# Optimization experiments

Hardware: AMD Instinct MI355X
Metric: run time of the kernel (lower is better)

The kernel has to match this reference:

```python
import jax, jax.numpy as jnp
import numpy as np

B, P, K = 32, 2048, 16
NHID, NCLS = 128, 10

def setup_inputs() -> dict:
    key = jax.random.key(0)
    ks = jax.random.split(key, 8)
    def w(k, shape):
        fan_in = shape[0]
        return jax.random.normal(k, shape, jnp.float32) / np.sqrt(fan_in)
    pos = jax.random.normal(ks[0], (B * P, 3), jnp.float32)
    batch = jnp.repeat(jnp.arange(B, dtype=jnp.int32), P)
    return dict(
        pos=pos, batch=batch,
        W1a=w(ks[1], (3 + 3, NHID)), b1a=jnp.zeros((NHID,), jnp.float32),
        W1b=w(ks[2], (NHID, NHID)), b1b=jnp.zeros((NHID,), jnp.float32),
        W2a=w(ks[3], (NHID + 3, NHID)), b2a=jnp.zeros((NHID,), jnp.float32),
        W2b=w(ks[4], (NHID, NHID)), b2b=jnp.zeros((NHID,), jnp.float32),
        Wc=w(ks[5], (NHID, NCLS)), bc=jnp.zeros((NCLS,), jnp.float32),
    )

def _gather(x, idx):
    # x: [B,P,C], idx: [B,P,K] -> [B,P,K,C]
    return jax.vmap(lambda xb, ib: xb[ib])(x, idx)

def _knn(posb):
    # posb: [B,P,3]; k nearest (incl. self, loop=True) per node -> [B,P,K]
    sq = jnp.sum(posb * posb, axis=-1)                      # [B,P]
    d2 = sq[:, :, None] + sq[:, None, :] - 2.0 * jnp.einsum('bpd,bqd->bpq', posb, posb)
    _, nbr = jax.lax.top_k(-d2, K)                          # [B,P,K]
    return nbr

def _pointnet_layer(h, posb, nbr, Wa, ba, Wb, bb):
    # message: concat(h_j, pos_j - pos_i) -> Linear -> ReLU -> Linear; aggr = max over K
    h_j = _gather(h, nbr)                                   # [B,P,K,C]
    rel = _gather(posb, nbr) - posb[:, :, None, :]          # [B,P,K,3]
    m = jnp.concatenate([h_j, rel], axis=-1)                # [B,P,K,C+3]
    m = jax.nn.relu(jnp.einsum('bpkc,cd->bpkd', m, Wa) + ba)
    m = jnp.einsum('bpkc,cd->bpkd', m, Wb) + bb
    return jnp.max(m, axis=2)                               # [B,P,NHID]

def reference(pos, batch, W1a, b1a, W1b, b1b, W2a, b2a, W2b, b2b, Wc, bc):
    posb = pos.reshape(B, P, 3)                             # batch is sorted, equal-size graphs
    nbr = _knn(posb)
    h = jax.nn.relu(_pointnet_layer(posb, posb, nbr, W1a, b1a, W1b, b1b))
    h = jax.nn.relu(_pointnet_layer(h, posb, nbr, W2a, b2a, W2b, b2b))
    g = jnp.max(h, axis=1)                                  # global_max_pool -> [B,NHID]
    return g @ Wc + bc                                      # [B,NCLS]
```

## Files before the change

kernel.cpp:

```cpp
#include <hip/hip_runtime.h>


typedef __bf16 bf16x8 __attribute__((ext_vector_type(8)));
typedef float  f32x4  __attribute__((ext_vector_type(4)));

#define LDSA __attribute__((aligned(16)))
#define WAVE_LDS_SYNC() __asm__ volatile("s_waitcnt lgkmcnt(0)" ::: "memory")

__global__ __launch_bounds__(512, 4) void knn_kernel(const float* __restrict__ pos,
                                                     int* __restrict__ nbr) {
  __shared__ LDSA float4 P4[2048];
  const int blk = blockIdx.x;
  const int b = blk >> 5;
  const int tid = threadIdx.x;
  const size_t bbase = (size_t)b * 2048;
  for (int idx = tid; idx < 2048; idx += 512) {
    const float* pp = pos + (bbase + idx) * 3;
    float x = pp[0], y = pp[1], z = pp[2];
    P4[idx] = make_float4(x, y, z, fmaf(z, z, fmaf(y, y, x * x)));
  }
  __syncthreads();
  const int wave = tid >> 6, lane = tid & 63;
  const int p0 = (blk & 31) * 64 + wave * 8;
  const unsigned long long below = (1ull << lane) - 1ull;
  const float FINF = __uint_as_float(0x7F800000u);
  for (int it = 0; it < 8; ++it) {
    const int pl = p0 + it;
    const float4 P = P4[pl];
    float m1 = FINF, m2 = FINF, m3 = FINF;
    unsigned s1 = 0, s2 = 0, s3 = 0;
#pragma unroll 8
    for (int i = 0; i < 32; ++i) {
      int c = lane + (i << 6);
      float4 Q = P4[c];
      float d2 = (P.w + Q.w) - 2.0f * fmaf(P.z, Q.z, fmaf(P.y, Q.y, P.x * Q.x));
      bool c3 = d2 < m3, c2 = d2 < m2, c1 = d2 < m1;
      m3 = c2 ? m2 : (c3 ? d2 : m3);  s3 = c2 ? s2 : (c3 ? (unsigned)c : s3);
      m2 = c1 ? m1 : (c2 ? d2 : m2);  s2 = c1 ? s1 : (c2 ? (unsigned)c : s2);
      m1 = c1 ? d2 : m1;              s1 = c1 ? (unsigned)c : s1;
    }
    unsigned k1 = __float_as_uint(m1); k1 = ((int)k1 < 0) ? ~k1 : (k1 | 0x80000000u);
    unsigned k2 = __float_as_uint(m2); k2 = ((int)k2 < 0) ? ~k2 : (k2 | 0x80000000u);
    unsigned k3 = __float_as_uint(m3); k3 = ((int)k3 < 0) ? ~k3 : (k3 | 0x80000000u);
    unsigned v = 0;
#pragma unroll
    for (int bit = 31; bit >= 0; --bit) {
      unsigned t = v | (1u << bit);
      int cnt = __popcll(__ballot(k1 < t)) + __popcll(__ballot(k2 < t)) +
                __popcll(__ballot(k3 < t));
      if (cnt < 16) v = t;
    }
    const unsigned V = v;
    const long long outbase = ((long long)bbase + pl) * 16;
    if (__any(k3 < V)) {
      unsigned long long K1 = ((unsigned long long)k1 << 32) | s1;
      unsigned long long K2 = ((unsigned long long)k2 << 32) | s2;
      unsigned long long K3 = ((unsigned long long)k3 << 32) | s3;
      unsigned long long lastk = 0;
      for (int r = 0; r < 16; ++r) {
        unsigned long long k = K1, kmin = K1;
#pragma unroll
        for (int off = 1; off < 64; off <<= 1) {
          unsigned long long o = __shfl_xor(kmin, off);
          kmin = (o < kmin) ? o : kmin;
        }
        if (lane == r) nbr[outbase + r] = (int)(kmin & 0xFFFFFFFFull);
        if (k == kmin) { lastk = k; K1 = K2; K2 = K3; K3 = ~0ull; }
        if (r < 15 && __any(K1 == ~0ull)) {
          if (K1 == ~0ull) {
            unsigned long long best = ~0ull;
            for (int i = 0; i < 32; ++i) {
              int c = lane + (i << 6);
              float4 Q = P4[c];
              float d2 = (P.w + Q.w) - 2.0f * fmaf(P.z, Q.z, fmaf(P.y, Q.y, P.x * Q.x));
              unsigned u = __float_as_uint(d2);
              u = ((int)u < 0) ? ~u : (u | 0x80000000u);
              unsigned long long kc = ((unsigned long long)u << 32) | (unsigned)c;
              bool ok = (kc > lastk) & (kc < best);
              best = ok ? kc : best;
            }
            K1 = best;
          }
        }
      }
    } else {
      unsigned long long L1 = __ballot(k1 < V), L2 = __ballot(k2 < V), L3 = __ballot(k3 < V);
      unsigned long long E1 = __ballot(k1 == V), E2 = __ballot(k2 == V), E3 = __ballot(k3 == V);
      int cA = __popcll(L1), cB = cA + __popcll(L2), cT = cB + __popcll(L3);
      int eA = __popcll(E1), eB = eA + __popcll(E2);
      {
        bool lt = k1 < V, eq = k1 == V;
        int plt = __popcll(L1 & below);
        int peq = cT + __popcll(E1 & below);
        int p = lt ? plt : peq;
        if (lt || (eq && peq < 16)) nbr[outbase + p] = (int)s1;
      }
      {
        bool lt = k2 < V, eq = k2 == V;
        int plt = cA + __popcll(L2 & below);
        int peq = cT + eA + __popcll(E2 & below);
        int p = lt ? plt : peq;
        if (lt || (eq && peq < 16)) nbr[outbase + p] = (int)s2;
      }
      {
        bool lt = k3 < V, eq = k3 == V;
        int plt = cB + __popcll(L3 & below);
        int peq = cT + eB + __popcll(E3 & below);
        int p = lt ? plt : peq;
        if (lt || (eq && peq < 16)) nbr[outbase + p] = (int)s3;
      }
    }
  }
}

__global__ __launch_bounds__(256, 2) void layer1_kernel(
    const float* __restrict__ pos, const int* __restrict__ nbr,
    const float* __restrict__ W1a, const float* __restrict__ b1a,
    const float* __restrict__ W1b, const float* __restrict__ b1b,
    __bf16* __restrict__ h1e) {
  __shared__ LDSA char smem[34816];
  __bf16* Wbt = (__bf16*)smem;
  const int tid = threadIdx.x;
  for (int idx = tid; idx < 16384; idx += 256) {
    int k = idx >> 7, n = idx & 127;
    Wbt[n * 136 + k] = (__bf16)W1b[idx];
  }
  __syncthreads();
  const int wave = tid >> 6, lane = tid & 63;
  const int q = lane >> 4, c15 = lane & 15;
  bf16x8 bfr[8][4];
#pragma unroll
  for (int nt = 0; nt < 8; ++nt)
#pragma unroll
    for (int t = 0; t < 4; ++t)
      bfr[nt][t] = *(const bf16x8*)&Wbt[(nt * 16 + c15) * 136 + t * 32 + q * 8];
  __syncthreads();
  __bf16* mt = (__bf16*)smem + wave * 2176;
  float* base = (float*)(smem + 17408) + wave * 128;
  const int cb = lane & 7, k0 = lane >> 3, C0 = cb * 16;
  float4 s0h[4], s1h[4], s2h[4];
#pragma unroll
  for (int i = 0; i < 4; ++i) {
    float4 a0 = *(const float4*)&W1a[      C0 + 4 * i], r0 = *(const float4*)&W1a[384 + C0 + 4 * i];
    float4 a1 = *(const float4*)&W1a[128 + C0 + 4 * i], r1 = *(const float4*)&W1a[512 + C0 + 4 * i];
    float4 a2 = *(const float4*)&W1a[256 + C0 + 4 * i], r2 = *(const float4*)&W1a[640 + C0 + 4 * i];
    s0h[i] = make_float4(a0.x + r0.x, a0.y + r0.y, a0.z + r0.z, a0.w + r0.w);
    s1h[i] = make_float4(a1.x + r1.x, a1.y + r1.y, a1.z + r1.z, a1.w + r1.w);
    s2h[i] = make_float4(a2.x + r2.x, a2.y + r2.y, a2.z + r2.z, a2.w + r2.w);
  }
  const int c2 = lane * 2;
  const float br0a = W1a[384 + c2], br0b = W1a[384 + c2 + 1];
  const float br1a = W1a[512 + c2], br1b = W1a[512 + c2 + 1];
  const float br2a = W1a[640 + c2], br2b = W1a[640 + c2 + 1];
  const float ba0 = b1a[c2], ba1 = b1a[c2 + 1];
  const float bbi0 = b1b[q * 32 + c15], bbi1 = b1b[q * 32 + 16 + c15];
  const int blk = blockIdx.x, b = blk >> 5;
  const size_t bbase = (size_t)b * 2048;
  const int p0 = (blk & 31) * 64 + wave * 16;
  size_t node = bbase + p0;
  int j0 = nbr[node * 16 + k0];
  int j1 = nbr[node * 16 + k0 + 8];
  float px = pos[node * 3], py = pos[node * 3 + 1], pz = pos[node * 3 + 2];
  for (int it = 0; it < 16; ++it) {
    const int j0c = j0, j1c = j1;
    const float xp = px, yp = py, zp = pz;
    const size_t nodec = node;
    if (it < 15) {
      node = nodec + 1;
      j0 = nbr[node * 16 + k0];
      j1 = nbr[node * 16 + k0 + 8];
      px = pos[node * 3]; py = pos[node * 3 + 1]; pz = pos[node * 3 + 2];
    }
    const float* pj0 = pos + (bbase + j0c) * 3;
    const float* pj1 = pos + (bbase + j1c) * 3;
    const float xa = pj0[0], ya = pj0[1], za = pj0[2];
    const float xb = pj1[0], yb = pj1[1], zb = pj1[2];
    float v0 = ba0 - fmaf(xp, br0a, fmaf(yp, br1a, zp * br2a));
    float v1 = ba1 - fmaf(xp, br0b, fmaf(yp, br1b, zp * br2b));
    *(float2*)&base[c2] = make_float2(v0, v1);
    WAVE_LDS_SYNC();
    float4 bb[4];
#pragma unroll
    for (int i = 0; i < 4; ++i) bb[i] = *(const float4*)&base[C0 + 4 * i];
#pragma unroll
    for (int r = 0; r < 2; ++r) {
      const float xj = r ? xb : xa, yj = r ? yb : ya, zj = r ? zb : za;
      bf16x8 o0, o1;
#pragma unroll
      for (int i = 0; i < 4; ++i) {
        float mx = fmaf(xj, s0h[i].x, fmaf(yj, s1h[i].x, fmaf(zj, s2h[i].x, bb[i].x)));
        float my = fmaf(xj, s0h[i].y, fmaf(yj, s1h[i].y, fmaf(zj, s2h[i].y, bb[i].y)));
        float mz = fmaf(xj, s0h[i].z, fmaf(yj, s1h[i].z, fmaf(zj, s2h[i].z, bb[i].z)));
        float mw = fmaf(xj, s0h[i].w, fmaf(yj, s1h[i].w, fmaf(zj, s2h[i].w, bb[i].w)));
        __bf16 e0 = (__bf16)fmaxf(mx, 0.f), e1 = (__bf16)fmaxf(my, 0.f);
        __bf16 e2 = (__bf16)fmaxf(mz, 0.f), e3 = (__bf16)fmaxf(mw, 0.f);
        if (i < 2) { o0[i * 4 + 0] = e0; o0[i * 4 + 1] = e1; o0[i * 4 + 2] = e2; o0[i * 4 + 3] = e3; }
        else { o1[(i - 2) * 4 + 0] = e0; o1[(i - 2) * 4 + 1] = e1; o1[(i - 2) * 4 + 2] = e2; o1[(i - 2) * 4 + 3] = e3; }
      }
      __bf16* dst = &mt[(k0 + 8 * r) * 136 + C0];
      *(bf16x8*)dst = o0;
      *(bf16x8*)(dst + 8) = o1;
    }
    WAVE_LDS_SYNC();
    bf16x8 af[4];
#pragma unroll
    for (int t = 0; t < 4; ++t)
      af[t] = *(const bf16x8*)&mt[c15 * 136 + t * 32 + q * 8];
    f32x4 acc[8] = {};
#pragma unroll
    for (int nt = 0; nt < 8; ++nt)
#pragma unroll
      for (int t = 0; t < 4; ++t)
        acc[nt] = __builtin_amdgcn_mfma_f32_16x16x32_bf16(af[t], bfr[nt][t], acc[nt], 0, 0, 0);
#pragma unroll
    for (int nt = 0; nt < 8; ++nt) {
      float m4 = fmaxf(fmaxf(acc[nt][0], acc[nt][1]), fmaxf(acc[nt][2], acc[nt][3]));
      m4 = fmaxf(m4, __shfl_xor(m4, 16));
      m4 = fmaxf(m4, __shfl_xor(m4, 32));
      if ((nt >> 1) == q) {
        float bias = (nt & 1) ? bbi1 : bbi0;
        h1e[nodec * 160 + nt * 16 + c15] = (__bf16)fmaxf(m4 + bias, 0.f);
      }
    }
    if (lane < 32) {
      __bf16 v = (__bf16)0.f;
      if (lane == 0) v = (__bf16)xp;
      else if (lane == 1) v = (__bf16)yp;
      else if (lane == 2) v = (__bf16)zp;
      h1e[nodec * 160 + 128 + lane] = v;
    }
  }
}

__global__ __launch_bounds__(256) void mid_gemm_kernel(
    const __bf16* __restrict__ h1e, const float* __restrict__ W2a,
    const float* __restrict__ b2a, __bf16* __restrict__ u2p) {
  __shared__ LDSA __bf16 Wt[128 * 168];
  const int tid = threadIdx.x;
  uint4 z = make_uint4(0, 0, 0, 0);
  for (int idx = tid; idx < 2688; idx += 256) ((uint4*)Wt)[idx] = z;
  __syncthreads();
  for (int idx = tid; idx < 131 * 32; idx += 256) {
    int k = idx >> 5, c4 = (idx & 31) * 4;
    float4 w = *(const float4*)&W2a[k * 128 + c4];
    Wt[(c4 + 0) * 168 + k] = (__bf16)w.x;
    Wt[(c4 + 1) * 168 + k] = (__bf16)w.y;
    Wt[(c4 + 2) * 168 + k] = (__bf16)w.z;
    Wt[(c4 + 3) * 168 + k] = (__bf16)w.w;
  }
  const int wave = tid >> 6, lane = tid & 63;
  const int q = lane >> 4, c15 = lane & 15;
  float biasr[8];
#pragma unroll
  for (int nt = 0; nt < 8; ++nt) biasr[nt] = b2a[nt * 16 + c15];
  __syncthreads();
  for (int tile = 0; tile < 4; ++tile) {
    const int row0 = blockIdx.x * 256 + tile * 64 + wave * 16;
    bf16x8 af[5];
#pragma unroll
    for (int t = 0; t < 5; ++t)
      af[t] = *(const bf16x8*)(h1e + (size_t)(row0 + c15) * 160 + t * 32 + q * 8);
    f32x4 acc[8] = {};
#pragma unroll
    for (int nt = 0; nt < 8; ++nt)
#pragma unroll
      for (int t = 0; t < 5; ++t) {
        bf16x8 bf = *(const bf16x8*)&Wt[(nt * 16 + c15) * 168 + t * 32 + q * 8];
        acc[nt] = __builtin_amdgcn_mfma_f32_16x16x32_bf16(af[t], bf, acc[nt], 0, 0, 0);
      }
#pragma unroll
    for (int nt = 0; nt < 8; ++nt) {
#pragma unroll
      for (int r = 0; r < 4; ++r)
        u2p[(size_t)(row0 + q * 4 + r) * 128 + nt * 16 + c15] = (__bf16)(acc[nt][r] + biasr[nt]);
    }
  }
}

__global__ __launch_bounds__(256, 2) void layer2_kernel(
    const float* __restrict__ pos, const int* __restrict__ nbr,
    const __bf16* __restrict__ u2p, const float* __restrict__ W2a,
    const float* __restrict__ W2b, const float* __restrict__ b2b,
    int* __restrict__ gG) {
  __shared__ LDSA char smem[34816];
  __shared__ int gpart[128];
  __bf16* Wbt = (__bf16*)smem;
  const int tid = threadIdx.x;
  for (int idx = tid; idx < 16384; idx += 256) {
    int k = idx >> 7, n = idx & 127;
    Wbt[n * 136 + k] = (__bf16)W2b[idx];
  }
  if (tid < 128) gpart[tid] = 0;
  __syncthreads();
  const int wave = tid >> 6, lane = tid & 63;
  const int q = lane >> 4, c15 = lane & 15;
  bf16x8 bfr[8][4];
#pragma unroll
  for (int nt = 0; nt < 8; ++nt)
#pragma unroll
    for (int t = 0; t < 4; ++t)
      bfr[nt][t] = *(const bf16x8*)&Wbt[(nt * 16 + c15) * 136 + t * 32 + q * 8];
  __syncthreads();
  __bf16* mt = (__bf16*)smem + wave * 2176;
  float* proj = (float*)(smem + 17408) + wave * 128;
  const int cb = lane & 7, k0 = lane >> 3, C0 = cb * 16;
  const int c2 = lane * 2;
  const float r0a = W2a[16384 + c2], r0b = W2a[16384 + c2 + 1];
  const float r1a = W2a[16512 + c2], r1b = W2a[16512 + c2 + 1];
  const float r2a = W2a[16640 + c2], r2b = W2a[16640 + c2 + 1];
  const float bbi0 = b2b[q * 32 + c15], bbi1 = b2b[q * 32 + 16 + c15];
  const int lb = blockIdx.x;
  const int xcd = lb & 7, slot = lb >> 3;
  const int b = xcd + 8 * (slot >> 5);
  const int bi = slot & 31;
  const size_t bbase = (size_t)b * 2048;
  const int p0 = bi * 64 + wave * 16;
  size_t node = bbase + p0;
  int j0 = nbr[node * 16 + k0];
  int j1 = nbr[node * 16 + k0 + 8];
  float px = pos[node * 3], py = pos[node * 3 + 1], pz = pos[node * 3 + 2];
  for (int it = 0; it < 16; ++it) {
    const int j0c = j0, j1c = j1;
    const float xp = px, yp = py, zp = pz;
    const size_t nodec = node;
    if (it < 15) {
      node = nodec + 1;
      j0 = nbr[node * 16 + k0];
      j1 = nbr[node * 16 + k0 + 8];
      px = pos[node * 3]; py = pos[node * 3 + 1]; pz = pos[node * 3 + 2];
    }
    const __bf16* ur0 = u2p + (size_t)(bbase + j0c) * 128 + C0;
    const __bf16* ur1 = u2p + (size_t)(bbase + j1c) * 128 + C0;
    bf16x8 ua0 = *(const bf16x8*)ur0, ua1 = *(const bf16x8*)(ur0 + 8);
    bf16x8 ub0 = *(const bf16x8*)ur1, ub1 = *(const bf16x8*)(ur1 + 8);
    float v0 = fmaf(xp, r0a, fmaf(yp, r1a, zp * r2a));
    float v1 = fmaf(xp, r0b, fmaf(yp, r1b, zp * r2b));
    *(float2*)&proj[c2] = make_float2(v0, v1);
    WAVE_LDS_SYNC();
    float pj[16];
#pragma unroll
    for (int i = 0; i < 4; ++i) *(float4*)&pj[4 * i] = *(const float4*)&proj[C0 + 4 * i];
#pragma unroll
    for (int r = 0; r < 2; ++r) {
      bf16x8 u0 = r ? ub0 : ua0, u1 = r ? ub1 : ua1;
      bf16x8 o0, o1;
#pragma unroll
      for (int e = 0; e < 8; ++e) o0[e] = (__bf16)fmaxf((float)u0[e] - pj[e], 0.f);
#pragma unroll
      for (int e = 0; e < 8; ++e) o1[e] = (__bf16)fmaxf((float)u1[e] - pj[8 + e], 0.f);
      __bf16* dst = &mt[(k0 + 8 * r) * 136 + C0];
      *(bf16x8*)dst = o0;
      *(bf16x8*)(dst + 8) = o1;
    }
    WAVE_LDS_SYNC();
    bf16x8 af[4];
#pragma unroll
    for (int t = 0; t < 4; ++t)
      af[t] = *(const bf16x8*)&mt[c15 * 136 + t * 32 + q * 8];
    f32x4 acc[8] = {};
#pragma unroll
    for (int nt = 0; nt < 8; ++nt)
#pragma unroll
      for (int t = 0; t < 4; ++t)
        acc[nt] = __builtin_amdgcn_mfma_f32_16x16x32_bf16(af[t], bfr[nt][t], acc[nt], 0, 0, 0);
#pragma unroll
    for (int nt = 0; nt < 8; ++nt) {
      float m4 = fmaxf(fmaxf(acc[nt][0], acc[nt][1]), fmaxf(acc[nt][2], acc[nt][3]));
      m4 = fmaxf(m4, __shfl_xor(m4, 16));
      m4 = fmaxf(m4, __shfl_xor(m4, 32));
      if ((nt >> 1) == q) {
        float bias = (nt & 1) ? bbi1 : bbi0;
        float h = fmaxf(m4 + bias, 0.f);
        atomicMax(&gpart[nt * 16 + c15], __float_as_int(h));
      }
    }
  }
  __syncthreads();
  if (tid < 128) atomicMax(&gG[b * 128 + tid], gpart[tid]);
}

__global__ __launch_bounds__(64) void cls_kernel(const int* __restrict__ gG,
                                                 const float* __restrict__ Wc,
                                                 const float* __restrict__ bc,
                                                 float* __restrict__ out) {
  const int b = blockIdx.x, lane = threadIdx.x;
  float g1 = __int_as_float(gG[b * 128 + lane]);
  float g2 = __int_as_float(gG[b * 128 + 64 + lane]);
  float accn[10];
#pragma unroll
  for (int n = 0; n < 10; ++n)
    accn[n] = g1 * Wc[lane * 10 + n] + g2 * Wc[(64 + lane) * 10 + n];
#pragma unroll
  for (int n = 0; n < 10; ++n) {
#pragma unroll
    for (int off = 32; off >= 1; off >>= 1) accn[n] += __shfl_xor(accn[n], off);
  }
  if (lane == 0) {
#pragma unroll
    for (int n = 0; n < 10; ++n) out[b * 10 + n] = accn[n] + bc[n];
  }
}

extern "C" void kernel_launch(void* const* d_in, const int* in_sizes, int n_in,
                              void* d_out, int out_size, void* d_ws, size_t ws_size,
                              hipStream_t stream) {
  const float* pos = (const float*)d_in[0];
  const float* W1a = (const float*)d_in[2];
  const float* b1a = (const float*)d_in[3];
  const float* W1b = (const float*)d_in[4];
  const float* b1b = (const float*)d_in[5];
  const float* W2a = (const float*)d_in[6];
  const float* b2a = (const float*)d_in[7];
  const float* W2b = (const float*)d_in[8];
  const float* b2b = (const float*)d_in[9];
  const float* Wc  = (const float*)d_in[10];
  const float* bc  = (const float*)d_in[11];

  char* ws = (char*)d_ws;
  int*    nbr = (int*)ws;
  __bf16* h1e = (__bf16*)(ws + 4194304);
  __bf16* u2p = (__bf16*)(ws + 25165824);
  int*    gG  = (int*)(ws + 41943040);
  float*  out = (float*)d_out;

  hipMemsetAsync(gG, 0, 32 * 128 * sizeof(int), stream);
  knn_kernel<<<1024, 512, 0, stream>>>(pos, nbr);
  layer1_kernel<<<1024, 256, 0, stream>>>(pos, nbr, W1a, b1a, W1b, b1b, h1e);
  mid_gemm_kernel<<<256, 256, 0, stream>>>(h1e, W2a, b2a, u2p);
  layer2_kernel<<<1024, 256, 0, stream>>>(pos, nbr, u2p, W2a, W2b, b2b, gG);
  cls_kernel<<<32, 64, 0, stream>>>(gG, Wc, bc, out);
}
```

Measured before the change: 350.8 us.

## Process four query points per kNN pass and prefetch neighbor gathers one iteration ahead

The kNN kernel now handles four query points at once, so each candidate float4 loaded from LDS is reused for four distance computations. The radix-select ballots for the four points are interleaved to overlap their latency, and the occupancy hint of 4 blocks is removed from the launch bounds. Both layer kernels now software-pipeline the dependent gather (neighbor positions in layer 1, projected features in layer 2) one iteration ahead instead of issuing it right after the index load. This trades more registers, and possibly lower occupancy, for less LDS traffic and more hidden memory latency.

Result: slower. 385.0 us (+9.8%).

```diff
diff --git a/kernel.cpp b/kernel.cpp
--- a/kernel.cpp
+++ b/kernel.cpp
@@ -7,8 +7,8 @@
 #define LDSA __attribute__((aligned(16)))
 #define WAVE_LDS_SYNC() __asm__ volatile("s_waitcnt lgkmcnt(0)" ::: "memory")
 
-__global__ __launch_bounds__(512, 4) void knn_kernel(const float* __restrict__ pos,
-                                                     int* __restrict__ nbr) {
+__global__ __launch_bounds__(512) void knn_kernel(const float* __restrict__ pos,
+                                                  int* __restrict__ nbr) {
   __shared__ LDSA float4 P4[2048];
   const int blk = blockIdx.x;
   const int b = blk >> 5;
@@ -24,90 +24,109 @@
   const int p0 = (blk & 31) * 64 + wave * 8;
   const unsigned long long below = (1ull << lane) - 1ull;
   const float FINF = __uint_as_float(0x7F800000u);
-  for (int it = 0; it < 8; ++it) {
-    const int pl = p0 + it;
-    const float4 P = P4[pl];
-    float m1 = FINF, m2 = FINF, m3 = FINF;
-    unsigned s1 = 0, s2 = 0, s3 = 0;
-#pragma unroll 8
+  for (int g = 0; g < 2; ++g) {
+    const int pb = p0 + g * 4;
+    float4 Pp[4];
+#pragma unroll
+    for (int p = 0; p < 4; ++p) Pp[p] = P4[pb + p];
+    float m1[4], m2[4], m3[4];
+    unsigned s1[4], s2[4], s3[4];
+#pragma unroll
+    for (int p = 0; p < 4; ++p) { m1[p] = m2[p] = m3[p] = FINF; s1[p] = s2[p] = s3[p] = 0; }
+#pragma unroll 2
     for (int i = 0; i < 32; ++i) {
       int c = lane + (i << 6);
       float4 Q = P4[c];
-      float d2 = (P.w + Q.w) - 2.0f * fmaf(P.z, Q.z, fmaf(P.y, Q.y, P.x * Q.x));
-      bool c3 = d2 < m3, c2 = d2 < m2, c1 = d2 < m1;
-      m3 = c2 ? m2 : (c3 ? d2 : m3);  s3 = c2 ? s2 : (c3 ? (unsigned)c : s3);
-      m2 = c1 ? m1 : (c2 ? d2 : m2);  s2 = c1 ? s1 : (c2 ? (unsigned)c : s2);
-      m1 = c1 ? d2 : m1;              s1 = c1 ? (unsigned)c : s1;
-    }
-    unsigned k1 = __float_as_uint(m1); k1 = ((int)k1 < 0) ? ~k1 : (k1 | 0x80000000u);
-    unsigned k2 = __float_as_uint(m2); k2 = ((int)k2 < 0) ? ~k2 : (k2 | 0x80000000u);
-    unsigned k3 = __float_as_uint(m3); k3 = ((int)k3 < 0) ? ~k3 : (k3 | 0x80000000u);
-    unsigned v = 0;
-#pragma unroll
+#pragma unroll
+      for (int p = 0; p < 4; ++p) {
+        float d2 = (Pp[p].w + Q.w) - 2.0f * fmaf(Pp[p].z, Q.z, fmaf(Pp[p].y, Q.y, Pp[p].x * Q.x));
+        bool c3 = d2 < m3[p], c2 = d2 < m2[p], c1 = d2 < m1[p];
+        m3[p] = c2 ? m2[p] : (c3 ? d2 : m3[p]);  s3[p] = c2 ? s2[p] : (c3 ? (unsigned)c : s3[p]);
+        m2[p] = c1 ? m1[p] : (c2 ? d2 : m2[p]);  s2[p] = c1 ? s1[p] : (c2 ? (unsigned)c : s2[p]);
+        m1[p] = c1 ? d2 : m1[p];                 s1[p] = c1 ? (unsigned)c : s1[p];
+      }
+    }
+    unsigned k1[4], k2[4], k3[4];
+#pragma unroll
+    for (int p = 0; p < 4; ++p) {
+      unsigned u;
+      u = __float_as_uint(m1[p]); k1[p] = ((int)u < 0) ? ~u : (u | 0x80000000u);
+      u = __float_as_uint(m2[p]); k2[p] = ((int)u < 0) ? ~u : (u | 0x80000000u);
+      u = __float_as_uint(m3[p]); k3[p] = ((int)u < 0) ? ~u : (u | 0x80000000u);
+    }
+    unsigned v[4] = {0, 0, 0, 0};
     for (int bit = 31; bit >= 0; --bit) {
-      unsigned t = v | (1u << bit);
-      int cnt = __popcll(__ballot(k1 < t)) + __popcll(__ballot(k2 < t)) +
-                __popcll(__ballot(k3 < t));
-      if (cnt < 16) v = t;
-    }
-    const unsigned V = v;
-    const long long outbase = ((long long)bbase + pl) * 16;
-    if (__any(k3 < V)) {
-      unsigned long long K1 = ((unsigned long long)k1 << 32) | s1;
-      unsigned long long K2 = ((unsigned long long)k2 << 32) | s2;
-      unsigned long long K3 = ((unsigned long long)k3 << 32) | s3;
-      unsigned long long lastk = 0;
-      for (int r = 0; r < 16; ++r) {
-        unsigned long long k = K1, kmin = K1;
-#pragma unroll
-        for (int off = 1; off < 64; off <<= 1) {
-          unsigned long long o = __shfl_xor(kmin, off);
-          kmin = (o < kmin) ? o : kmin;
-        }
-        if (lane == r) nbr[outbase + r] = (int)(kmin & 0xFFFFFFFFull);
-        if (k == kmin) { lastk = k; K1 = K2; K2 = K3; K3 = ~0ull; }
-        if (r < 15 && __any(K1 == ~0ull)) {
-          if (K1 == ~0ull) {
-            unsigned long long best = ~0ull;
-            for (int i = 0; i < 32; ++i) {
-              int c = lane + (i << 6);
-              float4 Q = P4[c];
-              float d2 = (P.w + Q.w) - 2.0f * fmaf(P.z, Q.z, fmaf(P.y, Q.y, P.x * Q.x));
-              unsigned u = __float_as_uint(d2);
-              u = ((int)u < 0) ? ~u : (u | 0x80000000u);
-              unsigned long long kc = ((unsigned long long)u << 32) | (unsigned)c;
-              bool ok = (kc > lastk) & (kc < best);
-              best = ok ? kc : best;
+      const unsigned msk = 1u << bit;
+#pragma unroll
+      for (int p = 0; p < 4; ++p) {
+        unsigned t = v[p] | msk;
+        int cnt = __popcll(__ballot(k1[p] < t)) + __popcll(__ballot(k2[p] < t)) +
+                  __popcll(__ballot(k3[p] < t));
+        if (cnt < 16) v[p] = t;
+      }
+    }
+#pragma unroll 1
+    for (int p = 0; p < 4; ++p) {
+      const unsigned V = v[p];
+      const long long outbase = ((long long)bbase + pb + p) * 16;
+      if (__any(k3[p] < V)) {
+        unsigned long long K1 = ((unsigned long long)k1[p] << 32) | s1[p];
+        unsigned long long K2 = ((unsigned long long)k2[p] << 32) | s2[p];
+        unsigned long long K3 = ((unsigned long long)k3[p] << 32) | s3[p];
+        unsigned long long lastk = 0;
+        const float4 P = Pp[p];
+        for (int r = 0; r < 16; ++r) {
+          unsigned long long k = K1, kmin = K1;
+#pragma unroll
+          for (int off = 1; off < 64; off <<= 1) {
+            unsigned long long o = __shfl_xor(kmin, off);
+            kmin = (o < kmin) ? o : kmin;
+          }
+          if (lane == r) nbr[outbase + r] = (int)(kmin & 0xFFFFFFFFull);
+          if (k == kmin) { lastk = k; K1 = K2; K2 = K3; K3 = ~0ull; }
+          if (r < 15 && __any(K1 == ~0ull)) {
+            if (K1 == ~0ull) {
+              unsigned long long best = ~0ull;
+              for (int i = 0; i < 32; ++i) {
+                int c = lane + (i << 6);
+                float4 Q = P4[c];
+                float d2 = (P.w + Q.w) - 2.0f * fmaf(P.z, Q.z, fmaf(P.y, Q.y, P.x * Q.x));
+                unsigned u = __float_as_uint(d2);
+                u = ((int)u < 0) ? ~u : (u | 0x80000000u);
+                unsigned long long kc = ((unsigned long long)u << 32) | (unsigned)c;
+                bool ok = (kc > lastk) & (kc < best);
+                best = ok ? kc : best;
+              }
+              K1 = best;
             }
-            K1 = best;
           }
         }
-      }
-    } else {
-      unsigned long long L1 = __ballot(k1 < V), L2 = __ballot(k2 < V), L3 = __ballot(k3 < V);
-      unsigned long long E1 = __ballot(k1 == V), E2 = __ballot(k2 == V), E3 = __ballot(k3 == V);
-      int cA = __popcll(L1), cB = cA + __popcll(L2), cT = cB + __popcll(L3);
-      int eA = __popcll(E1), eB = eA + __popcll(E2);
-      {
-        bool lt = k1 < V, eq = k1 == V;
-        int plt = __popcll(L1 & below);
-        int peq = cT + __popcll(E1 & below);
-        int p = lt ? plt : peq;
-        if (lt || (eq && peq < 16)) nbr[outbase + p] = (int)s1;
-      }
-      {
-        bool lt = k2 < V, eq = k2 == V;
-        int plt = cA + __popcll(L2 & below);
-        int peq = cT + eA + __popcll(E2 & below);
-        int p = lt ? plt : peq;
-        if (lt || (eq && peq < 16)) nbr[outbase + p] = (int)s2;
-      }
-      {
-        bool lt = k3 < V, eq = k3 == V;
-        int plt = cB + __popcll(L3 & below);
-        int peq = cT + eB + __popcll(E3 & below);
-        int p = lt ? plt : peq;
-        if (lt || (eq && peq < 16)) nbr[outbase + p] = (int)s3;
+      } else {
+        unsigned long long L1 = __ballot(k1[p] < V), L2 = __ballot(k2[p] < V), L3 = __ballot(k3[p] < V);
+        unsigned long long E1 = __ballot(k1[p] == V), E2 = __ballot(k2[p] == V), E3 = __ballot(k3[p] == V);
+        int cA = __popcll(L1), cB = cA + __popcll(L2), cT = cB + __popcll(L3);
+        int eA = __popcll(E1), eB = eA + __popcll(E2);
+        {
+          bool lt = k1[p] < V, eq = k1[p] == V;
+          int plt = __popcll(L1 & below);
+          int peq = cT + __popcll(E1 & below);
+          int pp2 = lt ? plt : peq;
+          if (lt || (eq && peq < 16)) nbr[outbase + pp2] = (int)s1[p];
+        }
+        {
+          bool lt = k2[p] < V, eq = k2[p] == V;
+          int plt = cA + __popcll(L2 & below);
+          int peq = cT + eA + __popcll(E2 & below);
+          int pp2 = lt ? plt : peq;
+          if (lt || (eq && peq < 16)) nbr[outbase + pp2] = (int)s2[p];
+        }
+        {
+          bool lt = k3[p] < V, eq = k3[p] == V;
+          int plt = cB + __popcll(L3 & below);
+          int peq = cT + eB + __popcll(E3 & below);
+          int pp2 = lt ? plt : peq;
+          if (lt || (eq && peq < 16)) nbr[outbase + pp2] = (int)s3[p];
+        }
       }
     }
   }
@@ -161,20 +180,25 @@
   int j0 = nbr[node * 16 + k0];
   int j1 = nbr[node * 16 + k0 + 8];
   float px = pos[node * 3], py = pos[node * 3 + 1], pz = pos[node * 3 + 2];
+  const float* t0 = pos + (bbase + j0) * 3;
+  const float* t1 = pos + (bbase + j1) * 3;
+  float xa = t0[0], ya = t0[1], za = t0[2];
+  float xb = t1[0], yb = t1[1], zb = t1[2];
   for (int it = 0; it < 16; ++it) {
-    const int j0c = j0, j1c = j1;
     const float xp = px, yp = py, zp = pz;
+    const float xac = xa, yac = ya, zac = za;
+    const float xbc = xb, ybc = yb, zbc = zb;
     const size_t nodec = node;
     if (it < 15) {
       node = nodec + 1;
       j0 = nbr[node * 16 + k0];
       j1 = nbr[node * 16 + k0 + 8];
       px = pos[node * 3]; py = pos[node * 3 + 1]; pz = pos[node * 3 + 2];
-    }
-    const float* pj0 = pos + (bbase + j0c) * 3;
-    const float* pj1 = pos + (bbase + j1c) * 3;
-    const float xa = pj0[0], ya = pj0[1], za = pj0[2];
-    const float xb = pj1[0], yb = pj1[1], zb = pj1[2];
+      const float* n0 = pos + (bbase + j0) * 3;
+      const float* n1 = pos + (bbase + j1) * 3;
+      xa = n0[0]; ya = n0[1]; za = n0[2];
+      xb = n1[0]; yb = n1[1]; zb = n1[2];
+    }
     float v0 = ba0 - fmaf(xp, br0a, fmaf(yp, br1a, zp * br2a));
     float v1 = ba1 - fmaf(xp, br0b, fmaf(yp, br1b, zp * br2b));
     *(float2*)&base[c2] = make_float2(v0, v1);
@@ -184,7 +208,7 @@
     for (int i = 0; i < 4; ++i) bb[i] = *(const float4*)&base[C0 + 4 * i];
 #pragma unroll
     for (int r = 0; r < 2; ++r) {
-      const float xj = r ? xb : xa, yj = r ? yb : ya, zj = r ? zb : za;
+      const float xj = r ? xbc : xac, yj = r ? ybc : yac, zj = r ? zbc : zac;
       bf16x8 o0, o1;
 #pragma unroll
       for (int i = 0; i < 4; ++i) {
@@ -319,20 +343,24 @@
   int j0 = nbr[node * 16 + k0];
   int j1 = nbr[node * 16 + k0 + 8];
   float px = pos[node * 3], py = pos[node * 3 + 1], pz = pos[node * 3 + 2];
+  const __bf16* g0 = u2p + (size_t)(bbase + j0) * 128 + C0;
+  const __bf16* g1 = u2p + (size_t)(bbase + j1) * 128 + C0;
+  bf16x8 ua0 = *(const bf16x8*)g0, ua1 = *(const bf16x8*)(g0 + 8);
+  bf16x8 ub0 = *(const bf16x8*)g1, ub1 = *(const bf16x8*)(g1 + 8);
   for (int it = 0; it < 16; ++it) {
-    const int j0c = j0, j1c = j1;
     const float xp = px, yp = py, zp = pz;
+    const bf16x8 ua0c = ua0, ua1c = ua1, ub0c = ub0, ub1c = ub1;
     const size_t nodec = node;
     if (it < 15) {
       node = nodec + 1;
       j0 = nbr[node * 16 + k0];
       j1 = nbr[node * 16 + k0 + 8];
       px = pos[node * 3]; py = pos[node * 3 + 1]; pz = pos[node * 3 + 2];
-    }
-    const __bf16* ur0 = u2p + (size_t)(bbase + j0c) * 128 + C0;
-    const __bf16* ur1 = u2p + (size_t)(bbase + j1c) * 128 + C0;
-    bf16x8 ua0 = *(const bf16x8*)ur0, ua1 = *(const bf16x8*)(ur0 + 8);
-    bf16x8 ub0 = *(const bf16x8*)ur1, ub1 = *(const bf16x8*)(ur1 + 8);
+      const __bf16* n0 = u2p + (size_t)(bbase + j0) * 128 + C0;
+      const __bf16* n1 = u2p + (size_t)(bbase + j1) * 128 + C0;
+      ua0 = *(const bf16x8*)n0; ua1 = *(const bf16x8*)(n0 + 8);
+      ub0 = *(const bf16x8*)n1; ub1 = *(const bf16x8*)(n1 + 8);
+    }
     float v0 = fmaf(xp, r0a, fmaf(yp, r1a, zp * r2a));
     float v1 = fmaf(xp, r0b, fmaf(yp, r1b, zp * r2b));
     *(float2*)&proj[c2] = make_float2(v0, v1);
@@ -342,7 +370,7 @@
     for (int i = 0; i < 4; ++i) *(float4*)&pj[4 * i] = *(const float4*)&proj[C0 + 4 * i];
 #pragma unroll
     for (int r = 0; r < 2; ++r) {
-      bf16x8 u0 = r ? ub0 : ua0, u1 = r ? ub1 : ua1;
+      bf16x8 u0 = r ? ub0c : ua0c, u1 = r ? ub1c : ua1c;
       bf16x8 o0, o1;
 #pragma unroll
       for (int e = 0; e < 8; ++e) o0[e] = (__bf16)fmaxf((float)u0[e] - pj[e], 0.f);
```

## Process two query points per kNN pass and prefetch neighbor gathers one iteration ahead

Applied to the files above, without the earlier changes.

The kNN kernel now handles two query points per scan of the shared position array, so each LDS load of a candidate is reused for two distance computations. The two radix-select loops are interleaved, and the fallback and emit paths are moved into helper functions. In both PointNet layer kernels, the gathered neighbor data (positions or u2p rows) is now loaded one node ahead, so the dependent gather latency overlaps with the current iteration's compute. The cost is higher register pressure from the doubled top-3 state and the prefetched values, which may reduce occupancy.

Result: slower. 388.8 us (+10.8%).

```diff
diff --git a/kernel.cpp b/kernel.cpp
--- a/kernel.cpp
+++ b/kernel.cpp
@@ -6,6 +6,73 @@
 
 #define LDSA __attribute__((aligned(16)))
 #define WAVE_LDS_SYNC() __asm__ volatile("s_waitcnt lgkmcnt(0)" ::: "memory")
+
+__device__ __forceinline__ void knn_emit_set(
+    unsigned V, unsigned k1, unsigned s1, unsigned k2, unsigned s2,
+    unsigned k3, unsigned s3, unsigned long long below,
+    int* __restrict__ nbr, long long outbase) {
+  unsigned long long L1 = __ballot(k1 < V), L2 = __ballot(k2 < V), L3 = __ballot(k3 < V);
+  unsigned long long E1 = __ballot(k1 == V), E2 = __ballot(k2 == V), E3 = __ballot(k3 == V);
+  int cA = __popcll(L1), cB = cA + __popcll(L2), cT = cB + __popcll(L3);
+  int eA = __popcll(E1), eB = eA + __popcll(E2);
+  {
+    bool lt = k1 < V, eq = k1 == V;
+    int plt = __popcll(L1 & below);
+    int peq = cT + __popcll(E1 & below);
+    int p = lt ? plt : peq;
+    if (lt || (eq && peq < 16)) nbr[outbase + p] = (int)s1;
+  }
+  {
+    bool lt = k2 < V, eq = k2 == V;
+    int plt = cA + __popcll(L2 & below);
+    int peq = cT + eA + __popcll(E2 & below);
+    int p = lt ? plt : peq;
+    if (lt || (eq && peq < 16)) nbr[outbase + p] = (int)s2;
+  }
+  {
+    bool lt = k3 < V, eq = k3 == V;
+    int plt = cB + __popcll(L3 & below);
+    int peq = cT + eB + __popcll(E3 & below);
+    int p = lt ? plt : peq;
+    if (lt || (eq && peq < 16)) nbr[outbase + p] = (int)s3;
+  }
+}
+
+__device__ __forceinline__ void knn_fallback(
+    const float4* __restrict__ P4, float4 P, int lane,
+    unsigned k1, unsigned s1, unsigned k2, unsigned s2, unsigned k3, unsigned s3,
+    int* __restrict__ nbr, long long outbase) {
+  unsigned long long K1 = ((unsigned long long)k1 << 32) | s1;
+  unsigned long long K2 = ((unsigned long long)k2 << 32) | s2;
+  unsigned long long K3 = ((unsigned long long)k3 << 32) | s3;
+  unsigned long long lastk = 0;
+  for (int r = 0; r < 16; ++r) {
+    unsigned long long k = K1, kmin = K1;
+#pragma unroll
+    for (int off = 1; off < 64; off <<= 1) {
+      unsigned long long o = __shfl_xor(kmin, off);
+      kmin = (o < kmin) ? o : kmin;
+    }
+    if (lane == r) nbr[outbase + r] = (int)(kmin & 0xFFFFFFFFull);
+    if (k == kmin) { lastk = k; K1 = K2; K2 = K3; K3 = ~0ull; }
+    if (r < 15 && __any(K1 == ~0ull)) {
+      if (K1 == ~0ull) {
+        unsigned long long best = ~0ull;
+        for (int i = 0; i < 32; ++i) {
+          int c = lane + (i << 6);
+          float4 Q = P4[c];
+          float d2 = (P.w + Q.w) - 2.0f * fmaf(P.z, Q.z, fmaf(P.y, Q.y, P.x * Q.x));
+          unsigned u = __float_as_uint(d2);
+          u = ((int)u < 0) ? ~u : (u | 0x80000000u);
+          unsigned long long kc = ((unsigned long long)u << 32) | (unsigned)c;
+          bool ok = (kc > lastk) & (kc < best);
+          best = ok ? kc : best;
+        }
+        K1 = best;
+      }
+    }
+  }
+}
 
 __global__ __launch_bounds__(512, 4) void knn_kernel(const float* __restrict__ pos,
                                                      int* __restrict__ nbr) {
@@ -24,92 +91,61 @@
   const int p0 = (blk & 31) * 64 + wave * 8;
   const unsigned long long below = (1ull << lane) - 1ull;
   const float FINF = __uint_as_float(0x7F800000u);
-  for (int it = 0; it < 8; ++it) {
-    const int pl = p0 + it;
-    const float4 P = P4[pl];
-    float m1 = FINF, m2 = FINF, m3 = FINF;
-    unsigned s1 = 0, s2 = 0, s3 = 0;
-#pragma unroll 8
+  for (int g = 0; g < 4; ++g) {
+    const int pA = p0 + g * 2;
+    const float4 Pa = P4[pA];
+    const float4 Pb = P4[pA + 1];
+    float m1a = FINF, m2a = FINF, m3a = FINF, m1b = FINF, m2b = FINF, m3b = FINF;
+    unsigned s1a = 0, s2a = 0, s3a = 0, s1b = 0, s2b = 0, s3b = 0;
+#pragma unroll 4
     for (int i = 0; i < 32; ++i) {
       int c = lane + (i << 6);
       float4 Q = P4[c];
-      float d2 = (P.w + Q.w) - 2.0f * fmaf(P.z, Q.z, fmaf(P.y, Q.y, P.x * Q.x));
-      bool c3 = d2 < m3, c2 = d2 < m2, c1 = d2 < m1;
-      m3 = c2 ? m2 : (c3 ? d2 : m3);  s3 = c2 ? s2 : (c3 ? (unsigned)c : s3);
-      m2 = c1 ? m1 : (c2 ? d2 : m2);  s2 = c1 ? s1 : (c2 ? (unsigned)c : s2);
-      m1 = c1 ? d2 : m1;              s1 = c1 ? (unsigned)c : s1;
-    }
-    unsigned k1 = __float_as_uint(m1); k1 = ((int)k1 < 0) ? ~k1 : (k1 | 0x80000000u);
-    unsigned k2 = __float_as_uint(m2); k2 = ((int)k2 < 0) ? ~k2 : (k2 | 0x80000000u);
-    unsigned k3 = __float_as_uint(m3); k3 = ((int)k3 < 0) ? ~k3 : (k3 | 0x80000000u);
-    unsigned v = 0;
-#pragma unroll
+      float da = (Pa.w + Q.w) - 2.0f * fmaf(Pa.z, Q.z, fmaf(Pa.y, Q.y, Pa.x * Q.x));
+      float db = (Pb.w + Q.w) - 2.0f * fmaf(Pb.z, Q.z, fmaf(Pb.y, Q.y, Pb.x * Q.x));
+      {
+        bool c3 = da < m3a, c2 = da < m2a, c1 = da < m1a;
+        m3a = c2 ? m2a : (c3 ? da : m3a);  s3a = c2 ? s2a : (c3 ? (unsigned)c : s3a);
+        m2a = c1 ? m1a : (c2 ? da : m2a);  s2a = c1 ? s1a : (c2 ? (unsigned)c : s2a);
+        m1a = c1 ? da : m1a;               s1a = c1 ? (unsigned)c : s1a;
+      }
+      {
+        bool c3 = db < m3b, c2 = db < m2b, c1 = db < m1b;
+        m3b = c2 ? m2b : (c3 ? db : m3b);  s3b = c2 ? s2b : (c3 ? (unsigned)c : s3b);
+        m2b = c1 ? m1b : (c2 ? db : m2b);  s2b = c1 ? s1b : (c2 ? (unsigned)c : s2b);
+        m1b = c1 ? db : m1b;               s1b = c1 ? (unsigned)c : s1b;
+      }
+    }
+    unsigned u;
+    unsigned k1a, k2a, k3a, k1b, k2b, k3b;
+    u = __float_as_uint(m1a); k1a = ((int)u < 0) ? ~u : (u | 0x80000000u);
+    u = __float_as_uint(m2a); k2a = ((int)u < 0) ? ~u : (u | 0x80000000u);
+    u = __float_as_uint(m3a); k3a = ((int)u < 0) ? ~u : (u | 0x80000000u);
+    u = __float_as_uint(m1b); k1b = ((int)u < 0) ? ~u : (u | 0x80000000u);
+    u = __float_as_uint(m2b); k2b = ((int)u < 0) ? ~u : (u | 0x80000000u);
+    u = __float_as_uint(m3b); k3b = ((int)u < 0) ? ~u : (u | 0x80000000u);
+    unsigned va = 0, vb = 0;
     for (int bit = 31; bit >= 0; --bit) {
-      unsigned t = v | (1u << bit);
-      int cnt = __popcll(__ballot(k1 < t)) + __popcll(__ballot(k2 < t)) +
-                __popcll(__ballot(k3 < t));
-      if (cnt < 16) v = t;
-    }
-    const unsigned V = v;
-    const long long outbase = ((long long)bbase + pl) * 16;
-    if (__any(k3 < V)) {
-      unsigned long long K1 = ((unsigned long long)k1 << 32) | s1;
-      unsigned long long K2 = ((unsigned long long)k2 << 32) | s2;
-      unsigned long long K3 = ((unsigned long long)k3 << 32) | s3;
-      unsigned long long lastk = 0;
-      for (int r = 0; r < 16; ++r) {
-        unsigned long long k = K1, kmin = K1;
-#pragma unroll
-        for (int off = 1; off < 64; off <<= 1) {
-          unsigned long long o = __shfl_xor(kmin, off);
-          kmin = (o < kmin) ? o : kmin;
-        }
-        if (lane == r) nbr[outbase + r] = (int)(kmin & 0xFFFFFFFFull);
-        if (k == kmin) { lastk = k; K1 = K2; K2 = K3; K3 = ~0ull; }
-        if (r < 15 && __any(K1 == ~0ull)) {
-          if (K1 == ~0ull) {
-            unsigned long long best = ~0ull;
-            for (int i = 0; i < 32; ++i) {
-              int c = lane + (i << 6);
-              float4 Q = P4[c];
-              float d2 = (P.w + Q.w) - 2.0f * fmaf(P.z, Q.z, fmaf(P.y, Q.y, P.x * Q.x));
-              unsigned u = __float_as_uint(d2);
-              u = ((int)u < 0) ? ~u : (u | 0x80000000u);
-              unsigned long long kc = ((unsigned long long)u << 32) | (unsigned)c;
-              bool ok = (kc > lastk) & (kc < best);
-              best = ok ? kc : best;
-            }
-            K1 = best;
-          }
-        }
-      }
-    } else {
-      unsigned long long L1 = __ballot(k1 < V), L2 = __ballot(k2 < V), L3 = __ballot(k3 < V);
-      unsigned long long E1 = __ballot(k1 == V), E2 = __ballot(k2 == V), E3 = __ballot(k3 == V);
-      int cA = __popcll(L1), cB = cA + __popcll(L2), cT = cB + __popcll(L3);
-      int eA = __popcll(E1), eB = eA + __popcll(E2);
-      {
-        bool lt = k1 < V, eq = k1 == V;
-        int plt = __popcll(L1 & below);
-        int peq = cT + __popcll(E1 & below);
-        int p = lt ? plt : peq;
-        if (lt || (eq && peq < 16)) nbr[outbase + p] = (int)s1;
-      }
-      {
-        bool lt = k2 < V, eq = k2 == V;
-        int plt = cA + __popcll(L2 & below);
-        int peq = cT + eA + __popcll(E2 & below);
-        int p = lt ? plt : peq;
-        if (lt || (eq && peq < 16)) nbr[outbase + p] = (int)s2;
-      }
-      {
-        bool lt = k3 < V, eq = k3 == V;
-        int plt = cB + __popcll(L3 & below);
-        int peq = cT + eB + __popcll(E3 & below);
-        int p = lt ? plt : peq;
-        if (lt || (eq && peq < 16)) nbr[outbase + p] = (int)s3;
-      }
-    }
+      const unsigned msk = 1u << bit;
+      unsigned ta = va | msk;
+      int ca = __popcll(__ballot(k1a < ta)) + __popcll(__ballot(k2a < ta)) +
+               __popcll(__ballot(k3a < ta));
+      if (ca < 16) va = ta;
+      unsigned tb = vb | msk;
+      int cb2 = __popcll(__ballot(k1b < tb)) + __popcll(__ballot(k2b < tb)) +
+                __popcll(__ballot(k3b < tb));
+      if (cb2 < 16) vb = tb;
+    }
+    const long long outA = ((long long)bbase + pA) * 16;
+    const long long outB = outA + 16;
+    if (__any(k3a < va))
+      knn_fallback(P4, Pa, lane, k1a, s1a, k2a, s2a, k3a, s3a, nbr, outA);
+    else
+      knn_emit_set(va, k1a, s1a, k2a, s2a, k3a, s3a, below, nbr, outA);
+    if (__any(k3b < vb))
+      knn_fallback(P4, Pb, lane, k1b, s1b, k2b, s2b, k3b, s3b, nbr, outB);
+    else
+      knn_emit_set(vb, k1b, s1b, k2b, s2b, k3b, s3b, below, nbr, outB);
   }
 }
 
@@ -161,20 +197,25 @@
   int j0 = nbr[node * 16 + k0];
   int j1 = nbr[node * 16 + k0 + 8];
   float px = pos[node * 3], py = pos[node * 3 + 1], pz = pos[node * 3 + 2];
+  const float* t0 = pos + (bbase + j0) * 3;
+  const float* t1 = pos + (bbase + j1) * 3;
+  float xa = t0[0], ya = t0[1], za = t0[2];
+  float xb = t1[0], yb = t1[1], zb = t1[2];
   for (int it = 0; it < 16; ++it) {
-    const int j0c = j0, j1c = j1;
     const float xp = px, yp = py, zp = pz;
+    const float xac = xa, yac = ya, zac = za;
+    const float xbc = xb, ybc = yb, zbc = zb;
     const size_t nodec = node;
     if (it < 15) {
       node = nodec + 1;
       j0 = nbr[node * 16 + k0];
       j1 = nbr[node * 16 + k0 + 8];
       px = pos[node * 3]; py = pos[node * 3 + 1]; pz = pos[node * 3 + 2];
-    }
-    const float* pj0 = pos + (bbase + j0c) * 3;
-    const float* pj1 = pos + (bbase + j1c) * 3;
-    const float xa = pj0[0], ya = pj0[1], za = pj0[2];
-    const float xb = pj1[0], yb = pj1[1], zb = pj1[2];
+      const float* n0 = pos + (bbase + j0) * 3;
+      const float* n1 = pos + (bbase + j1) * 3;
+      xa = n0[0]; ya = n0[1]; za = n0[2];
+      xb = n1[0]; yb = n1[1]; zb = n1[2];
+    }
     float v0 = ba0 - fmaf(xp, br0a, fmaf(yp, br1a, zp * br2a));
     float v1 = ba1 - fmaf(xp, br0b, fmaf(yp, br1b, zp * br2b));
     *(float2*)&base[c2] = make_float2(v0, v1);
@@ -184,7 +225,7 @@
     for (int i = 0; i < 4; ++i) bb[i] = *(const float4*)&base[C0 + 4 * i];
 #pragma unroll
     for (int r = 0; r < 2; ++r) {
-      const float xj = r ? xb : xa, yj = r ? yb : ya, zj = r ? zb : za;
+      const float xj = r ? xbc : xac, yj = r ? ybc : yac, zj = r ? zbc : zac;
       bf16x8 o0, o1;
 #pragma unroll
       for (int i = 0; i < 4; ++i) {
@@ -319,20 +360,24 @@
   int j0 = nbr[node * 16 + k0];
   int j1 = nbr[node * 16 + k0 + 8];
   float px = pos[node * 3], py = pos[node * 3 + 1], pz = pos[node * 3 + 2];
+  const __bf16* g0 = u2p + (size_t)(bbase + j0) * 128 + C0;
+  const __bf16* g1 = u2p + (size_t)(bbase + j1) * 128 + C0;
+  bf16x8 ua0 = *(const bf16x8*)g0, ua1 = *(const bf16x8*)(g0 + 8);
+  bf16x8 ub0 = *(const bf16x8*)g1, ub1 = *(const bf16x8*)(g1 + 8);
   for (int it = 0; it < 16; ++it) {
-    const int j0c = j0, j1c = j1;
     const float xp = px, yp = py, zp = pz;
+    const bf16x8 ua0c = ua0, ua1c = ua1, ub0c = ub0, ub1c = ub1;
     const size_t nodec = node;
     if (it < 15) {
       node = nodec + 1;
       j0 = nbr[node * 16 + k0];
       j1 = nbr[node * 16 + k0 + 8];
       px = pos[node * 3]; py = pos[node * 3 + 1]; pz = pos[node * 3 + 2];
-    }
-    const __bf16* ur0 = u2p + (size_t)(bbase + j0c) * 128 + C0;
-    const __bf16* ur1 = u2p + (size_t)(bbase + j1c) * 128 + C0;
-    bf16x8 ua0 = *(const bf16x8*)ur0, ua1 = *(const bf16x8*)(ur0 + 8);
-    bf16x8 ub0 = *(const bf16x8*)ur1, ub1 = *(const bf16x8*)(ur1 + 8);
+      const __bf16* n0 = u2p + (size_t)(bbase + j0) * 128 + C0;
+      const __bf16* n1 = u2p + (size_t)(bbase + j1) * 128 + C0;
+      ua0 = *(const bf16x8*)n0; ua1 = *(const bf16x8*)(n0 + 8);
+      ub0 = *(const bf16x8*)n1; ub1 = *(const bf16x8*)(n1 + 8);
+    }
     float v0 = fmaf(xp, r0a, fmaf(yp, r1a, zp * r2a));
     float v1 = fmaf(xp, r0b, fmaf(yp, r1b, zp * r2b));
     *(float2*)&proj[c2] = make_float2(v0, v1);
@@ -342,7 +387,7 @@
     for (int i = 0; i < 4; ++i) *(float4*)&pj[4 * i] = *(const float4*)&proj[C0 + 4 * i];
 #pragma unroll
     for (int r = 0; r < 2; ++r) {
-      bf16x8 u0 = r ? ub0 : ua0, u1 = r ? ub1 : ua1;
+      bf16x8 u0 = r ? ub0c : ua0c, u1 = r ? ub1c : ua1c;
       bf16x8 o0, o1;
 #pragma unroll
       for (int e = 0; e < 8; ++e) o0[e] = (__bf16)fmaxf((float)u0[e] - pj[e], 0.f);
```

## Simplify kNN distance with med3 top-3 and prefetch gathered neighbor data

Applied to the files above, without the earlier changes.

The kNN kernel now stores -2*pos in LDS so each candidate distance is three chained FMAs, dropping the separate |p|^2 term, which is constant per query row and so leaves the ranking unchanged. The running top-3 minimum update uses fmed3/fmin instead of nested selects, and the launch_bounds min-occupancy hint is removed. In both pointnet layers, the dependent gather of neighbor positions and neighbor feature rows is software-pipelined one node ahead, so those loads overlap the current iteration's compute. This adds register pressure, and the distance values change numerically, which could reorder near-ties.

New measurement: 362.6 us. 1.03x slower.

```diff
diff --git a/kernel.cpp b/kernel.cpp
--- a/kernel.cpp
+++ b/kernel.cpp
@@ -7,8 +7,8 @@
 #define LDSA __attribute__((aligned(16)))
 #define WAVE_LDS_SYNC() __asm__ volatile("s_waitcnt lgkmcnt(0)" ::: "memory")
 
-__global__ __launch_bounds__(512, 4) void knn_kernel(const float* __restrict__ pos,
-                                                     int* __restrict__ nbr) {
+__global__ __launch_bounds__(512) void knn_kernel(const float* __restrict__ pos,
+                                                  int* __restrict__ nbr) {
   __shared__ LDSA float4 P4[2048];
   const int blk = blockIdx.x;
   const int b = blk >> 5;
@@ -17,7 +17,7 @@
   for (int idx = tid; idx < 2048; idx += 512) {
     const float* pp = pos + (bbase + idx) * 3;
     float x = pp[0], y = pp[1], z = pp[2];
-    P4[idx] = make_float4(x, y, z, fmaf(z, z, fmaf(y, y, x * x)));
+    P4[idx] = make_float4(-2.0f * x, -2.0f * y, -2.0f * z, fmaf(z, z, fmaf(y, y, x * x)));
   }
   __syncthreads();
   const int wave = tid >> 6, lane = tid & 63;
@@ -26,22 +26,29 @@
   const float FINF = __uint_as_float(0x7F800000u);
   for (int it = 0; it < 8; ++it) {
     const int pl = p0 + it;
-    const float4 P = P4[pl];
+    const float4 Qp = P4[pl];
+    const float Px = -0.5f * Qp.x, Py = -0.5f * Qp.y, Pz = -0.5f * Qp.z;
     float m1 = FINF, m2 = FINF, m3 = FINF;
     unsigned s1 = 0, s2 = 0, s3 = 0;
 #pragma unroll 8
     for (int i = 0; i < 32; ++i) {
       int c = lane + (i << 6);
       float4 Q = P4[c];
-      float d2 = (P.w + Q.w) - 2.0f * fmaf(P.z, Q.z, fmaf(P.y, Q.y, P.x * Q.x));
-      bool c3 = d2 < m3, c2 = d2 < m2, c1 = d2 < m1;
-      m3 = c2 ? m2 : (c3 ? d2 : m3);  s3 = c2 ? s2 : (c3 ? (unsigned)c : s3);
-      m2 = c1 ? m1 : (c2 ? d2 : m2);  s2 = c1 ? s1 : (c2 ? (unsigned)c : s2);
-      m1 = c1 ? d2 : m1;              s1 = c1 ? (unsigned)c : s1;
-    }
-    unsigned k1 = __float_as_uint(m1); k1 = ((int)k1 < 0) ? ~k1 : (k1 | 0x80000000u);
-    unsigned k2 = __float_as_uint(m2); k2 = ((int)k2 < 0) ? ~k2 : (k2 | 0x80000000u);
-    unsigned k3 = __float_as_uint(m3); k3 = ((int)k3 < 0) ? ~k3 : (k3 | 0x80000000u);
+      float d2 = fmaf(Px, Q.x, fmaf(Py, Q.y, fmaf(Pz, Q.z, Q.w)));
+      bool c1 = d2 < m1, c2 = d2 < m2, c3 = d2 < m3;
+      float n3 = __builtin_amdgcn_fmed3f(d2, m2, m3);
+      float n2 = __builtin_amdgcn_fmed3f(d2, m1, m2);
+      float n1 = fminf(d2, m1);
+      s3 = c2 ? s2 : (c3 ? (unsigned)c : s3);
+      s2 = c1 ? s1 : (c2 ? (unsigned)c : s2);
+      s1 = c1 ? (unsigned)c : s1;
+      m1 = n1; m2 = n2; m3 = n3;
+    }
+    unsigned u;
+    unsigned k1, k2, k3;
+    u = __float_as_uint(m1); k1 = ((int)u < 0) ? ~u : (u | 0x80000000u);
+    u = __float_as_uint(m2); k2 = ((int)u < 0) ? ~u : (u | 0x80000000u);
+    u = __float_as_uint(m3); k3 = ((int)u < 0) ? ~u : (u | 0x80000000u);
     unsigned v = 0;
 #pragma unroll
     for (int bit = 31; bit >= 0; --bit) {
@@ -72,10 +79,10 @@
             for (int i = 0; i < 32; ++i) {
               int c = lane + (i << 6);
               float4 Q = P4[c];
-              float d2 = (P.w + Q.w) - 2.0f * fmaf(P.z, Q.z, fmaf(P.y, Q.y, P.x * Q.x));
-              unsigned u = __float_as_uint(d2);
-              u = ((int)u < 0) ? ~u : (u | 0x80000000u);
-              unsigned long long kc = ((unsigned long long)u << 32) | (unsigned)c;
+              float d2 = fmaf(Px, Q.x, fmaf(Py, Q.y, fmaf(Pz, Q.z, Q.w)));
+              unsigned uu = __float_as_uint(d2);
+              uu = ((int)uu < 0) ? ~uu : (uu | 0x80000000u);
+              unsigned long long kc = ((unsigned long long)uu << 32) | (unsigned)c;
               bool ok = (kc > lastk) & (kc < best);
               best = ok ? kc : best;
             }
@@ -161,20 +168,25 @@
   int j0 = nbr[node * 16 + k0];
   int j1 = nbr[node * 16 + k0 + 8];
   float px = pos[node * 3], py = pos[node * 3 + 1], pz = pos[node * 3 + 2];
+  const float* t0 = pos + (bbase + j0) * 3;
+  const float* t1 = pos + (bbase + j1) * 3;
+  float xa = t0[0], ya = t0[1], za = t0[2];
+  float xb = t1[0], yb = t1[1], zb = t1[2];
   for (int it = 0; it < 16; ++it) {
-    const int j0c = j0, j1c = j1;
     const float xp = px, yp = py, zp = pz;
+    const float xac = xa, yac = ya, zac = za;
+    const float xbc = xb, ybc = yb, zbc = zb;
     const size_t nodec = node;
     if (it < 15) {
       node = nodec + 1;
       j0 = nbr[node * 16 + k0];
       j1 = nbr[node * 16 + k0 + 8];
       px = pos[node * 3]; py = pos[node * 3 + 1]; pz = pos[node * 3 + 2];
-    }
-    const float* pj0 = pos + (bbase + j0c) * 3;
-    const float* pj1 = pos + (bbase + j1c) * 3;
-    const float xa = pj0[0], ya = pj0[1], za = pj0[2];
-    const float xb = pj1[0], yb = pj1[1], zb = pj1[2];
+      const float* n0 = pos + (bbase + j0) * 3;
+      const float* n1 = pos + (bbase + j1) * 3;
+      xa = n0[0]; ya = n0[1]; za = n0[2];
+      xb = n1[0]; yb = n1[1]; zb = n1[2];
+    }
     float v0 = ba0 - fmaf(xp, br0a, fmaf(yp, br1a, zp * br2a));
     float v1 = ba1 - fmaf(xp, br0b, fmaf(yp, br1b, zp * br2b));
     *(float2*)&base[c2] = make_float2(v0, v1);
@@ -184,7 +196,7 @@
     for (int i = 0; i < 4; ++i) bb[i] = *(const float4*)&base[C0 + 4 * i];
 #pragma unroll
     for (int r = 0; r < 2; ++r) {
-      const float xj = r ? xb : xa, yj = r ? yb : ya, zj = r ? zb : za;
+      const float xj = r ? xbc : xac, yj = r ? ybc : yac, zj = r ? zbc : zac;
       bf16x8 o0, o1;
 #pragma unroll
       for (int i = 0; i < 4; ++i) {
@@ -319,20 +331,24 @@
   int j0 = nbr[node * 16 + k0];
   int j1 = nbr[node * 16 + k0 + 8];
   float px = pos[node * 3], py = pos[node * 3 + 1], pz = pos[node * 3 + 2];
+  const __bf16* g0 = u2p + (size_t)(bbase + j0) * 128 + C0;
+  const __bf16* g1 = u2p + (size_t)(bbase + j1) * 128 + C0;
+  bf16x8 ua0 = *(const bf16x8*)g0, ua1 = *(const bf16x8*)(g0 + 8);
+  bf16x8 ub0 = *(const bf16x8*)g1, ub1 = *(const bf16x8*)(g1 + 8);
   for (int it = 0; it < 16; ++it) {
-    const int j0c = j0, j1c = j1;
     const float xp = px, yp = py, zp = pz;
+    const bf16x8 ua0c = ua0, ua1c = ua1, ub0c = ub0, ub1c = ub1;
     const size_t nodec = node;
     if (it < 15) {
       node = nodec + 1;
       j0 = nbr[node * 16 + k0];
       j1 = nbr[node * 16 + k0 + 8];
       px = pos[node * 3]; py = pos[node * 3 + 1]; pz = pos[node * 3 + 2];
-    }
-    const __bf16* ur0 = u2p + (size_t)(bbase + j0c) * 128 + C0;
-    const __bf16* ur1 = u2p + (size_t)(bbase + j1c) * 128 + C0;
-    bf16x8 ua0 = *(const bf16x8*)ur0, ua1 = *(const bf16x8*)(ur0 + 8);
-    bf16x8 ub0 = *(const bf16x8*)ur1, ub1 = *(const bf16x8*)(ur1 + 8);
+      const __bf16* n0 = u2p + (size_t)(bbase + j0) * 128 + C0;
+      const __bf16* n1 = u2p + (size_t)(bbase + j1) * 128 + C0;
+      ua0 = *(const bf16x8*)n0; ua1 = *(const bf16x8*)(n0 + 8);
+      ub0 = *(const bf16x8*)n1; ub1 = *(const bf16x8*)(n1 + 8);
+    }
     float v0 = fmaf(xp, r0a, fmaf(yp, r1a, zp * r2a));
     float v1 = fmaf(xp, r0b, fmaf(yp, r1b, zp * r2b));
     *(float2*)&proj[c2] = make_float2(v0, v1);
@@ -342,7 +358,7 @@
     for (int i = 0; i < 4; ++i) *(float4*)&pj[4 * i] = *(const float4*)&proj[C0 + 4 * i];
 #pragma unroll
     for (int r = 0; r < 2; ++r) {
-      bf16x8 u0 = r ? ub0 : ua0, u1 = r ? ub1 : ua1;
+      bf16x8 u0 = r ? ub0c : ua0c, u1 = r ? ub1c : ua1c;
       bf16x8 o0, o1;
 #pragma unroll
       for (int e = 0; e < 8; ++e) o0[e] = (__bf16)fmaxf((float)u0[e] - pj[e], 0.f);
```
